# Kernel tuning notes

Hardware: AMD Instinct MI355X
Metric: run time of the kernel (lower is better)

Reference implementation:

```python
import jax, jax.numpy as jnp
import numpy as np

D_MODEL = 2048
D_INNER = 2048
D_XB = 512
N_HEADS = 32
HEADDIM = 64   # P
DSTATE = 64    # N
N_KV = D_XB // DSTATE          # 8 kv heads
REP = N_HEADS // N_KV
D_FF = 8192
DCONV = 4
EPS = 1e-5
B, L = 1, 2048


def _rmsnorm(x, w, eps=EPS):
    return x * jax.lax.rsqrt(jnp.mean(x * x, axis=-1, keepdims=True) + eps) * w


def _silu(x):
    return x * jax.nn.sigmoid(x)


def _causal_dwconv(x, w, b):
    # x: (B,L,C), depthwise causal conv, kernel DCONV
    xp = jnp.pad(x, ((0, 0), (DCONV - 1, 0), (0, 0)))
    y = b
    for k in range(DCONV):  # small fixed kernel loop
        y = y + xp[:, k:k + x.shape[1], :] * w[:, k]
    return y


def setup_inputs() -> dict:
    key = jax.random.key(0)
    ks = jax.random.split(key, 10)
    s = 0.02
    d_proj = 2 * D_INNER + 2 * D_XB + N_HEADS  # z, x, B, C, dt
    conv_ch = 2 * D_XB + D_INNER               # conv over concat(x, B, C)
    return {
        "hidden_states": jax.random.normal(ks[0], (B, L, D_MODEL), jnp.float32),
        "in_proj_w": jax.random.normal(ks[1], (d_proj, D_MODEL), jnp.float32) * s,
        "conv_w": jax.random.normal(ks[2], (conv_ch, DCONV), jnp.float32) * s,
        "conv_b": jnp.zeros((conv_ch,), jnp.float32),
        "dt_bias": jax.random.normal(ks[3], (N_HEADS,), jnp.float32) * s,
        "A_log": jnp.log(jnp.arange(1, N_HEADS + 1, dtype=jnp.float32)),
        "D": jnp.ones((N_HEADS,), jnp.float32),
        "ssm_norm_w": jnp.ones((D_INNER,), jnp.float32),
        "out_proj_w": jax.random.normal(ks[4], (D_MODEL, D_INNER), jnp.float32) * s,
        "input_ln_w": jnp.ones((D_MODEL,), jnp.float32),
        "post_ln_w": jnp.ones((D_MODEL,), jnp.float32),
        "gate_w": jax.random.normal(ks[5], (D_FF, D_MODEL), jnp.float32) * s,
        "up_w": jax.random.normal(ks[6], (D_FF, D_MODEL), jnp.float32) * s,
        "down_w": jax.random.normal(ks[7], (D_MODEL, D_FF), jnp.float32) * s,
    }


def _mamba2(hs, in_proj_w, conv_w, conv_b, dt_bias, A_log, D, ssm_norm_w, out_proj_w):
    b, l, _ = hs.shape
    zxbcdt = hs @ in_proj_w.T
    z, x, Bm, Cm, dt = jnp.split(
        zxbcdt, [D_INNER, D_INNER + D_XB, D_INNER + 2 * D_XB, 2 * D_INNER + 2 * D_XB], axis=-1)
    # causal depthwise conv + silu over concat(x, B, C)
    xBC = _silu(_causal_dwconv(jnp.concatenate([x, Bm, Cm], axis=-1), conv_w, conv_b))
    x, Bm, Cm = jnp.split(xBC, [D_XB, 2 * D_XB], axis=-1)
    # heads (GQA: repeat x and B from N_KV to N_HEADS)
    x = jnp.repeat(x.reshape(b, l, N_KV, HEADDIM), REP, axis=2)      # (b,l,H,P)
    Bm = jnp.repeat(Bm.reshape(b, l, N_KV, DSTATE), REP, axis=2)     # (b,l,H,N)
    Cm = Cm.reshape(b, l, N_HEADS, DSTATE)                            # (b,l,H,N)
    dt = jax.nn.softplus(dt + dt_bias)                                # (b,l,H)
    dA = jnp.exp(dt * (-jnp.exp(A_log)))                              # (b,l,H)
    # selective scan over time
    xs = (jnp.moveaxis(dA, 1, 0), jnp.moveaxis(dt, 1, 0),
          jnp.moveaxis(x, 1, 0), jnp.moveaxis(Bm, 1, 0), jnp.moveaxis(Cm, 1, 0))
    h0 = jnp.zeros((b, N_HEADS, HEADDIM, DSTATE), hs.dtype)

    def step(h, t):
        dA_t, dt_t, x_t, B_t, C_t = t
        h = h * dA_t[:, :, None, None] + jnp.einsum('bh,bhp,bhn->bhpn', dt_t, x_t, B_t)
        y = jnp.einsum('bhpn,bhn->bhp', h, C_t)
        return h, y

    _, ys = jax.lax.scan(step, h0, xs)            # (l,b,H,P)
    y = jnp.moveaxis(ys, 0, 1) + D[None, None, :, None] * x
    y = y.reshape(b, l, D_INNER)
    y = _rmsnorm(y * _silu(z), ssm_norm_w)        # gated RMSNorm
    return y @ out_proj_w.T


def reference(hidden_states, in_proj_w, conv_w, conv_b, dt_bias, A_log, D,
              ssm_norm_w, out_proj_w, input_ln_w, post_ln_w, gate_w, up_w, down_w):
    residual = hidden_states
    h = _rmsnorm(hidden_states, input_ln_w)
    h = residual + _mamba2(h, in_proj_w, conv_w, conv_b, dt_bias, A_log, D,
                           ssm_norm_w, out_proj_w)
    residual = h
    h = _rmsnorm(h, post_ln_w)
    h = (_silu(h @ gate_w.T) * (h @ up_w.T)) @ down_w.T
    return residual + h
```

## Files before the change

kernel.cpp:

```cpp
#include <hip/hip_runtime.h>

typedef unsigned short u16;
typedef unsigned int u32;
typedef float f32x4 __attribute__((ext_vector_type(4)));
typedef __bf16 bf16x8 __attribute__((ext_vector_type(8)));
typedef unsigned short u16x8 __attribute__((ext_vector_type(8)));

#define L_SEQ 2048
#define DMODEL 2048
#define DINNER 2048
#define DXB 512
#define NHEADS 32
#define DPROJ 5152
#define CONVCH 3072
#define DFF 8192
#define NCHUNK 32
#define CHUNK 64

__device__ __forceinline__ float bf2f(u16 u) {
  union { unsigned int i; float f; } v; v.i = ((unsigned int)u) << 16; return v.f;
}
__device__ __forceinline__ u16 f2bf(float f) {
  union { float f; unsigned int i; } v; v.f = f;
  unsigned int u = v.i;
  u += 0x7FFFu + ((u >> 16) & 1u);
  return (u16)(u >> 16);
}
__device__ __forceinline__ float siluf(float x) { return x / (1.f + __expf(-x)); }

#define GL16(gsrc, ldst) \
  __builtin_amdgcn_global_load_lds((const __attribute__((address_space(1))) u32*)(gsrc), \
                                   (__attribute__((address_space(3))) u32*)(ldst), 16, 0, 0)

__global__ __launch_bounds__(256) void cvt_k(
    const float* __restrict__ s, u16* __restrict__ d, int n8)
{
  const int i = blockIdx.x * 256 + threadIdx.x;
  if (i >= n8) return;
  f32x4 a = *(const f32x4*)(s + (size_t)i * 8);
  f32x4 b = *(const f32x4*)(s + (size_t)i * 8 + 4);
  u16x8 o;
#pragma unroll
  for (int j = 0; j < 4; ++j) { o[j] = f2bf(a[j]); o[j + 4] = f2bf(b[j]); }
  *(u16x8*)(d + (size_t)i * 8) = o;
}

template<int EPI, int SPLIT>
__global__ __launch_bounds__(256, 4) void gemm_gl(
    const u16* __restrict__ A, const u16* __restrict__ W,
    void* Cptr, const u16* gateB, int N, int K)
{
  __shared__ u16 Al[128 * 64];
  __shared__ u16 Bl[128 * 64];
  const int tid = threadIdx.x;
  const int w = tid >> 6, ln = tid & 63;
  const int m0 = blockIdx.y << 7, n0 = blockIdx.x << 7;
  const int steps = (K >> 6) / SPLIT;
  const int kt0 = blockIdx.z * steps;

  const int lrow = ln >> 3;
  const int lcol = (ln & 7) << 3;

  f32x4 acc[4][4];
#pragma unroll
  for (int i = 0; i < 4; ++i)
#pragma unroll
    for (int j = 0; j < 4; ++j) acc[i][j] = f32x4{0.f, 0.f, 0.f, 0.f};

  const int wr = w >> 1, wc = w & 1;
  const int lr = ln & 15;
  const int lk = (ln >> 4) << 3;

  for (int kt = kt0; kt < kt0 + steps; ++kt) {
    const int kc = (kt << 6) + lcol;
#pragma unroll
    for (int i = 0; i < 4; ++i) {
      const int r = w * 32 + i * 8;
      GL16(A + (size_t)(m0 + r + lrow) * K + kc, &Al[r * 64]);
      int rw = n0 + r + lrow; rw = rw < N ? rw : N - 1;
      GL16(W + (size_t)rw * K + kc, &Bl[r * 64]);
    }
    __syncthreads();
    bf16x8 af[4], bfr[4];
#pragma unroll
    for (int kk = 0; kk < 2; ++kk) {
#pragma unroll
      for (int m = 0; m < 4; ++m)
        af[m] = *(const bf16x8*)&Al[(wr * 64 + m * 16 + lr) * 64 + kk * 32 + lk];
#pragma unroll
      for (int n = 0; n < 4; ++n)
        bfr[n] = *(const bf16x8*)&Bl[(wc * 64 + n * 16 + lr) * 64 + kk * 32 + lk];
#pragma unroll
      for (int m = 0; m < 4; ++m)
#pragma unroll
        for (int n = 0; n < 4; ++n)
          acc[m][n] = __builtin_amdgcn_mfma_f32_16x16x32_bf16(af[m], bfr[n], acc[m][n], 0, 0, 0);
    }
    __syncthreads();
  }

  const int colb = n0 + (wc << 6) + lr;
  const int rowb = m0 + (wr << 6) + ((ln >> 4) << 2);
#pragma unroll
  for (int m = 0; m < 4; ++m) {
#pragma unroll
    for (int n = 0; n < 4; ++n) {
      const int col = colb + (n << 4);
      if (col < N) {
#pragma unroll
        for (int j = 0; j < 4; ++j) {
          const size_t idx = (size_t)(rowb + (m << 4) + j) * N + col;
          if (EPI == 0) {
            ((u16*)Cptr)[idx] = f2bf(acc[m][n][j]);
          } else if (EPI == 2) {
            float* P = (float*)Cptr + (size_t)blockIdx.z * ((size_t)L_SEQ * N);
            P[idx] = acc[m][n][j];
          } else {
            const float g = bf2f(gateB[idx]);
            ((u16*)Cptr)[idx] = f2bf(siluf(g) * acc[m][n][j]);
          }
        }
      }
    }
  }
}

__global__ __launch_bounds__(256) void rmsnorm_k(
    const float* __restrict__ in, const float* __restrict__ w, u16* __restrict__ out)
{
  const int row = blockIdx.x, tid = threadIdx.x;
  const float* r = in + (size_t)row * DMODEL + tid * 8;
  f32x4 v0 = *(const f32x4*)r;
  f32x4 v1 = *(const f32x4*)(r + 4);
  float ss = v0[0]*v0[0] + v0[1]*v0[1] + v0[2]*v0[2] + v0[3]*v0[3]
           + v1[0]*v1[0] + v1[1]*v1[1] + v1[2]*v1[2] + v1[3]*v1[3];
#pragma unroll
  for (int off = 1; off < 64; off <<= 1) ss += __shfl_xor(ss, off);
  __shared__ float part[4];
  if ((tid & 63) == 0) part[tid >> 6] = ss;
  __syncthreads();
  const float tot = part[0] + part[1] + part[2] + part[3];
  const float scale = rsqrtf(tot * (1.f / DMODEL) + 1e-5f);
  f32x4 w0 = *(const f32x4*)(w + tid * 8);
  f32x4 w1 = *(const f32x4*)(w + tid * 8 + 4);
  u16x8 o;
#pragma unroll
  for (int j = 0; j < 4; ++j) {
    o[j]     = f2bf(v0[j] * scale * w0[j]);
    o[j + 4] = f2bf(v1[j] * scale * w1[j]);
  }
  *(u16x8*)(out + (size_t)row * DMODEL + tid * 8) = o;
}

__global__ __launch_bounds__(256) void red4_rms_k(
    const float* __restrict__ P, const float* __restrict__ resid,
    float* __restrict__ hres, const float* __restrict__ w, u16* __restrict__ h2)
{
  const int row = blockIdx.x, tid = threadIdx.x;
  const size_t base = (size_t)row * DMODEL + tid * 8;
  const size_t stride = (size_t)L_SEQ * DMODEL;
  f32x4 v0 = *(const f32x4*)(resid + base);
  f32x4 v1 = *(const f32x4*)(resid + base + 4);
#pragma unroll
  for (int p = 0; p < 4; ++p) {
    v0 += *(const f32x4*)(P + p * stride + base);
    v1 += *(const f32x4*)(P + p * stride + base + 4);
  }
  *(f32x4*)(hres + base) = v0;
  *(f32x4*)(hres + base + 4) = v1;
  float ss = v0[0]*v0[0] + v0[1]*v0[1] + v0[2]*v0[2] + v0[3]*v0[3]
           + v1[0]*v1[0] + v1[1]*v1[1] + v1[2]*v1[2] + v1[3]*v1[3];
#pragma unroll
  for (int off = 1; off < 64; off <<= 1) ss += __shfl_xor(ss, off);
  __shared__ float part[4];
  if ((tid & 63) == 0) part[tid >> 6] = ss;
  __syncthreads();
  const float tot = part[0] + part[1] + part[2] + part[3];
  const float scale = rsqrtf(tot * (1.f / DMODEL) + 1e-5f);
  f32x4 w0 = *(const f32x4*)(w + tid * 8);
  f32x4 w1 = *(const f32x4*)(w + tid * 8 + 4);
  u16x8 o;
#pragma unroll
  for (int j = 0; j < 4; ++j) {
    o[j]     = f2bf(v0[j] * scale * w0[j]);
    o[j + 4] = f2bf(v1[j] * scale * w1[j]);
  }
  *(u16x8*)(h2 + base) = o;
}

__global__ __launch_bounds__(256) void red4_add_k(
    const float* __restrict__ P, const float* __restrict__ resid, float* __restrict__ out)
{
  const size_t base = ((size_t)blockIdx.x * 256 + threadIdx.x) * 8;
  const size_t stride = (size_t)L_SEQ * DMODEL;
  f32x4 v0 = *(const f32x4*)(resid + base);
  f32x4 v1 = *(const f32x4*)(resid + base + 4);
#pragma unroll
  for (int p = 0; p < 4; ++p) {
    v0 += *(const f32x4*)(P + p * stride + base);
    v1 += *(const f32x4*)(P + p * stride + base + 4);
  }
  *(f32x4*)(out + base) = v0;
  *(f32x4*)(out + base + 4) = v1;
}

__global__ __launch_bounds__(256) void gated_rms_k(
    const float* __restrict__ y, const u16* __restrict__ zx,
    const float* __restrict__ w, u16* __restrict__ out)
{
  const int row = blockIdx.x, tid = threadIdx.x;
  const float* yr = y + (size_t)row * DINNER + tid * 8;
  f32x4 y0 = *(const f32x4*)yr;
  f32x4 y1 = *(const f32x4*)(yr + 4);
  u16x8 zv = *(const u16x8*)(zx + (size_t)row * DPROJ + tid * 8);
  float val[8];
#pragma unroll
  for (int j = 0; j < 4; ++j) {
    val[j]     = y0[j] * siluf(bf2f(zv[j]));
    val[j + 4] = y1[j] * siluf(bf2f(zv[j + 4]));
  }
  float ss = 0.f;
#pragma unroll
  for (int j = 0; j < 8; ++j) ss += val[j] * val[j];
#pragma unroll
  for (int off = 1; off < 64; off <<= 1) ss += __shfl_xor(ss, off);
  __shared__ float part[4];
  if ((tid & 63) == 0) part[tid >> 6] = ss;
  __syncthreads();
  const float tot = part[0] + part[1] + part[2] + part[3];
  const float scale = rsqrtf(tot * (1.f / DINNER) + 1e-5f);
  u16x8 o;
#pragma unroll
  for (int j = 0; j < 8; ++j) o[j] = f2bf(val[j] * scale * w[tid * 8 + j]);
  *(u16x8*)(out + (size_t)row * DINNER + tid * 8) = o;
}

__global__ __launch_bounds__(256) void conv_k(
    const u16* __restrict__ zx, const float* __restrict__ w,
    const float* __restrict__ b, u16* __restrict__ xbc)
{
  const int flat = blockIdx.x * 256 + threadIdx.x;
  const int t = flat / 384;
  const int c8 = (flat % 384) * 8;
  float acc[8];
  f32x4 b0 = *(const f32x4*)(b + c8);
  f32x4 b1 = *(const f32x4*)(b + c8 + 4);
#pragma unroll
  for (int j = 0; j < 4; ++j) { acc[j] = b0[j]; acc[j + 4] = b1[j]; }
  f32x4 wr[8];
#pragma unroll
  for (int j = 0; j < 8; ++j) wr[j] = *(const f32x4*)(w + (size_t)(c8 + j) * 4);
#pragma unroll
  for (int k = 0; k < 4; ++k) {
    const int tt = t - 3 + k;
    if (tt >= 0) {
      u16x8 xv = *(const u16x8*)(zx + (size_t)tt * DPROJ + DINNER + c8);
#pragma unroll
      for (int j = 0; j < 8; ++j) acc[j] += bf2f(xv[j]) * wr[j][k];
    }
  }
  u16x8 o;
#pragma unroll
  for (int j = 0; j < 8; ++j) o[j] = f2bf(siluf(acc[j]));
  *(u16x8*)(xbc + (size_t)t * CONVCH + c8) = o;
}

__global__ __launch_bounds__(256) void dt_k(
    const u16* __restrict__ zx, const float* __restrict__ dt_bias,
    const float* __restrict__ A_log, float* __restrict__ dtv, float* __restrict__ dAv)
{
  const int flat = blockIdx.x * 256 + threadIdx.x;
  const int t = flat >> 5, h = flat & 31;
  const float x = bf2f(zx[(size_t)t * DPROJ + (DPROJ - NHEADS) + h]) + dt_bias[h];
  const float sp = (x > 20.f) ? x : log1pf(expf(x));
  const float a = expf(A_log[h]);
  dtv[flat] = sp;
  dAv[flat] = expf(-a * sp);
}

__device__ __forceinline__ void stage16(float* dst, const u16* src) {
  u16x8 a = *(const u16x8*)src;
  u16x8 b = *(const u16x8*)(src + 8);
#pragma unroll
  for (int j = 0; j < 8; ++j) { dst[j] = bf2f(a[j]); dst[8 + j] = bf2f(b[j]); }
}

__global__ __launch_bounds__(256) void scan_a(
    const u16* __restrict__ xbc, const float* __restrict__ dtv,
    const float* __restrict__ dAv, const float* __restrict__ Dvec,
    float* __restrict__ y, float* __restrict__ S,
    float* __restrict__ gam, float* __restrict__ cum)
{
  __shared__ float xs[64][64], Bs[64][64], Cs[64][64];
  __shared__ float dts[64], dAs[64];
  const int c = blockIdx.x, h = blockIdx.y, kv = h >> 2;
  const int tid = threadIdx.x;
  const int t0 = c * CHUNK;
  {
    const int r = tid >> 2, cq = (tid & 3) * 16;
    const u16* base = xbc + (size_t)(t0 + r) * CONVCH;
    stage16(&xs[r][cq], base + kv * 64 + cq);
    stage16(&Bs[r][cq], base + DXB + kv * 64 + cq);
    stage16(&Cs[r][cq], base + 2 * DXB + h * 64 + cq);
    if (tid < 64) {
      dts[tid] = dtv[(size_t)(t0 + tid) * NHEADS + h];
      dAs[tid] = dAv[(size_t)(t0 + tid) * NHEADS + h];
    }
  }
  __syncthreads();
  const int p = tid >> 2, q = tid & 3;
  float hreg[16];
#pragma unroll
  for (int i = 0; i < 16; ++i) hreg[i] = 0.f;
  float cumv = 1.f;
  const float Dh = Dvec[h];
  for (int t = 0; t < CHUNK; ++t) {
    const float dtt = dts[t], dat = dAs[t];
    const float xv = xs[t][p];
    const float u = dtt * xv;
    float a0 = 0.f, a1 = 0.f, a2 = 0.f, a3 = 0.f;
#pragma unroll
    for (int i4 = 0; i4 < 4; ++i4) {
      f32x4 b4 = *(const f32x4*)&Bs[t][q * 16 + i4 * 4];
      f32x4 c4 = *(const f32x4*)&Cs[t][q * 16 + i4 * 4];
#pragma unroll
      for (int j = 0; j < 4; ++j) {
        const int i = i4 * 4 + j;
        hreg[i] = hreg[i] * dat + u * b4[j];
        if (i4 == 0) a0 += hreg[i] * c4[j];
        else if (i4 == 1) a1 += hreg[i] * c4[j];
        else if (i4 == 2) a2 += hreg[i] * c4[j];
        else a3 += hreg[i] * c4[j];
      }
    }
    float accv = (a0 + a1) + (a2 + a3);
    accv += __shfl_xor(accv, 1);
    accv += __shfl_xor(accv, 2);
    cumv *= dat;
    if (q == 0) y[(size_t)(t0 + t) * DINNER + h * 64 + p] = accv + Dh * xv;
    if (tid == 0) cum[(size_t)(t0 + t) * NHEADS + h] = cumv;
  }
  float* Sp = S + ((size_t)(c * NHEADS + h) << 12) + tid * 16;
#pragma unroll
  for (int i4 = 0; i4 < 4; ++i4)
    *(f32x4*)(Sp + i4 * 4) = f32x4{hreg[i4*4], hreg[i4*4+1], hreg[i4*4+2], hreg[i4*4+3]};
  if (tid == 0) gam[c * NHEADS + h] = cumv;
}

__global__ __launch_bounds__(256) void scan_b(
    const float* __restrict__ S, const float* __restrict__ gam, float* __restrict__ H)
{
  const int h = blockIdx.x, tid = threadIdx.x;
  float hr[16];
#pragma unroll
  for (int i = 0; i < 16; ++i) hr[i] = 0.f;
  for (int c = 0; c < NCHUNK; ++c) {
    const size_t base = ((size_t)(c * NHEADS + h) << 12) + tid * 16;
#pragma unroll
    for (int i4 = 0; i4 < 4; ++i4)
      *(f32x4*)(H + base + i4 * 4) = f32x4{hr[i4*4], hr[i4*4+1], hr[i4*4+2], hr[i4*4+3]};
    const float g = gam[c * NHEADS + h];
#pragma unroll
    for (int i4 = 0; i4 < 4; ++i4) {
      f32x4 s = *(const f32x4*)(S + base + i4 * 4);
#pragma unroll
      for (int j = 0; j < 4; ++j) hr[i4 * 4 + j] = g * hr[i4 * 4 + j] + s[j];
    }
  }
}

__global__ __launch_bounds__(256) void scan_c(
    const u16* __restrict__ xbc, const float* __restrict__ cum,
    const float* __restrict__ H, float* __restrict__ y)
{
  __shared__ float Cs[64][64];
  __shared__ float cums[64];
  const int c = blockIdx.x, h = blockIdx.y, tid = threadIdx.x;
  const int t0 = c * CHUNK;
  {
    const int r = tid >> 2, cq = (tid & 3) * 16;
    stage16(&Cs[r][cq], xbc + (size_t)(t0 + r) * CONVCH + 2 * DXB + h * 64 + cq);
    if (tid < 64) cums[tid] = cum[(size_t)(t0 + tid) * NHEADS + h];
  }
  const int p = tid >> 2, q = tid & 3;
  float hr[16];
  const size_t base = ((size_t)(c * NHEADS + h) << 12) + tid * 16;
#pragma unroll
  for (int i4 = 0; i4 < 4; ++i4) {
    f32x4 v = *(const f32x4*)(H + base + i4 * 4);
#pragma unroll
    for (int j = 0; j < 4; ++j) hr[i4 * 4 + j] = v[j];
  }
  __syncthreads();
  for (int t = 0; t < CHUNK; ++t) {
    float accv = 0.f;
#pragma unroll
    for (int i4 = 0; i4 < 4; ++i4) {
      f32x4 c4 = *(const f32x4*)&Cs[t][q * 16 + i4 * 4];
#pragma unroll
      for (int j = 0; j < 4; ++j) accv += hr[i4 * 4 + j] * c4[j];
    }
    accv += __shfl_xor(accv, 1);
    accv += __shfl_xor(accv, 2);
    if (q == 0) {
      const size_t idx = (size_t)(t0 + t) * DINNER + h * 64 + p;
      y[idx] += cums[t] * accv;
    }
  }
}

extern "C" void kernel_launch(void* const* d_in, const int* in_sizes, int n_in,
                              void* d_out, int out_size, void* d_ws, size_t ws_size,
                              hipStream_t stream) {
  const float* hs         = (const float*)d_in[0];
  const float* in_proj_w  = (const float*)d_in[1];
  const float* conv_w     = (const float*)d_in[2];
  const float* conv_b     = (const float*)d_in[3];
  const float* dt_bias    = (const float*)d_in[4];
  const float* A_log      = (const float*)d_in[5];
  const float* Dv         = (const float*)d_in[6];
  const float* ssm_w      = (const float*)d_in[7];
  const float* out_proj_w = (const float*)d_in[8];
  const float* in_ln_w    = (const float*)d_in[9];
  const float* post_ln_w  = (const float*)d_in[10];
  const float* gate_w     = (const float*)d_in[11];
  const float* up_w       = (const float*)d_in[12];
  const float* down_w     = (const float*)d_in[13];
  float* out = (float*)d_out;

  char* ws = (char*)d_ws;
  size_t off = 0;
  auto alloc = [&](size_t bytes) -> void* {
    void* p = ws + off;
    off = (off + bytes + 255) & ~(size_t)255;
    return p;
  };
  u16* wip = (u16*)alloc((size_t)DPROJ  * DMODEL * 2);
  u16* wop = (u16*)alloc((size_t)DMODEL * DINNER * 2);
  u16* wg  = (u16*)alloc((size_t)DFF    * DMODEL * 2);
  u16* wu  = (u16*)alloc((size_t)DFF    * DMODEL * 2);
  u16* wd  = (u16*)alloc((size_t)DMODEL * DFF    * 2);
  u16*   zx  = (u16*)  alloc((size_t)L_SEQ * DPROJ * 2);
  u16*   xbc = (u16*)  alloc((size_t)L_SEQ * CONVCH * 2);
  float* Sv  = (float*)alloc((size_t)NCHUNK * NHEADS * 4096 * 4);
  float* Hv  = (float*)alloc((size_t)NCHUNK * NHEADS * 4096 * 4);
  float* pK  = (float*)zx;
  float* dtv = (float*)alloc((size_t)L_SEQ * NHEADS * 4);
  float* dAv = (float*)alloc((size_t)L_SEQ * NHEADS * 4);
  float* cum = (float*)alloc((size_t)L_SEQ * NHEADS * 4);
  float* gam = (float*)alloc((size_t)NCHUNK * NHEADS * 4);
  float* yv  = (float*)alloc((size_t)L_SEQ * DINNER * 4);
  float* hres= (float*)alloc((size_t)L_SEQ * DMODEL * 4);
  u16*  gateb= (u16*)  alloc((size_t)L_SEQ * DFF * 2);
  u16*  hslot= (u16*)  alloc((size_t)L_SEQ * DMODEL * 2);
  (void)ws_size; (void)in_sizes; (void)n_in; (void)out_size;

  cvt_k<<<(DPROJ * DMODEL / 8 + 255) / 256, 256, 0, stream>>>(in_proj_w, wip, DPROJ * DMODEL / 8);
  cvt_k<<<DMODEL * DINNER / 8 / 256, 256, 0, stream>>>(out_proj_w, wop, DMODEL * DINNER / 8);
  cvt_k<<<DFF * DMODEL / 8 / 256, 256, 0, stream>>>(gate_w, wg, DFF * DMODEL / 8);
  cvt_k<<<DFF * DMODEL / 8 / 256, 256, 0, stream>>>(up_w, wu, DFF * DMODEL / 8);
  cvt_k<<<DMODEL * DFF / 8 / 256, 256, 0, stream>>>(down_w, wd, DMODEL * DFF / 8);

  rmsnorm_k<<<L_SEQ, 256, 0, stream>>>(hs, in_ln_w, hslot);
  gemm_gl<0, 1><<<dim3(41, 16, 1), 256, 0, stream>>>(hslot, wip, zx, nullptr, DPROJ, DMODEL);
  conv_k<<<(L_SEQ * (CONVCH / 8)) / 256, 256, 0, stream>>>(zx, conv_w, conv_b, xbc);
  dt_k<<<(L_SEQ * NHEADS) / 256, 256, 0, stream>>>(zx, dt_bias, A_log, dtv, dAv);
  scan_a<<<dim3(NCHUNK, NHEADS), 256, 0, stream>>>(xbc, dtv, dAv, Dv, yv, Sv, gam, cum);
  scan_b<<<NHEADS, 256, 0, stream>>>(Sv, gam, Hv);
  scan_c<<<dim3(NCHUNK, NHEADS), 256, 0, stream>>>(xbc, cum, Hv, yv);
  gated_rms_k<<<L_SEQ, 256, 0, stream>>>(yv, zx, ssm_w, hslot);
  gemm_gl<2, 4><<<dim3(16, 16, 4), 256, 0, stream>>>(hslot, wop, pK, nullptr, DMODEL, DINNER);
  red4_rms_k<<<L_SEQ, 256, 0, stream>>>(pK, hs, hres, post_ln_w, hslot);
  gemm_gl<0, 1><<<dim3(64, 16, 1), 256, 0, stream>>>(hslot, wg, gateb, nullptr, DFF, DMODEL);
  gemm_gl<3, 1><<<dim3(64, 16, 1), 256, 0, stream>>>(hslot, wu, gateb, gateb, DFF, DMODEL);
  gemm_gl<2, 4><<<dim3(16, 16, 4), 256, 0, stream>>>(gateb, wd, pK, nullptr, DMODEL, DFF);
  red4_add_k<<<(L_SEQ * DMODEL / 8) / 256, 256, 0, stream>>>(pK, hres, out);
}
```

Before: 604.5 us.

## Replace GEMM with 256x256 double-buffered 8-wave pipelined kernel

Replaces the 128x128 single-buffered GEMM with a 256x256-tile, 512-thread kernel. It double-buffers LDS with global_load_lds, swizzles LDS columns to avoid bank conflicts, interleaves quarter-tile MFMA bursts with the next stage's loads using explicit waitcnt, barriers and setprio, and remaps workgroups across XCDs. The in_proj weight is zero-padded to a multiple of 256 rows so the loader needs no clamping. The aim is to hide global-load latency and raise MFMA utilisation in the GEMMs that dominate runtime. The cost is a large LDS footprint, lower occupancy, and fewer workgroups for the smaller GEMMs, which risks under-filling the GPU.

```diff
diff --git a/kernel.cpp b/kernel.cpp
--- a/kernel.cpp
+++ b/kernel.cpp
@@ -12,6 +12,7 @@
 #define DXB 512
 #define NHEADS 32
 #define DPROJ 5152
+#define DPROJ_PAD 5376
 #define CONVCH 3072
 #define DFF 8192
 #define NCHUNK 32
@@ -31,6 +32,11 @@
 #define GL16(gsrc, ldst) \
   __builtin_amdgcn_global_load_lds((const __attribute__((address_space(1))) u32*)(gsrc), \
                                    (__attribute__((address_space(3))) u32*)(ldst), 16, 0, 0)
+#define SBAR() __builtin_amdgcn_s_barrier()
+#define SCHED0() __builtin_amdgcn_sched_barrier(0)
+#define WAIT_LGKM0() do { asm volatile("s_waitcnt lgkmcnt(0)" ::: "memory"); SCHED0(); } while (0)
+#define WAIT_VM4() asm volatile("s_waitcnt vmcnt(4)" ::: "memory")
+#define WAIT_VM0() asm volatile("s_waitcnt vmcnt(0)" ::: "memory")
 
 __global__ __launch_bounds__(256) void cvt_k(
     const float* __restrict__ s, u16* __restrict__ d, int n8)
@@ -45,79 +51,185 @@
   *(u16x8*)(d + (size_t)i * 8) = o;
 }
 
+__global__ __launch_bounds__(256) void cvt_pad_k(
+    const float* __restrict__ s, u16* __restrict__ d)
+{
+  const int i = blockIdx.x * 256 + threadIdx.x;
+  const int row = (i * 8) >> 11;
+  u16x8 o;
+  if (row < DPROJ) {
+    f32x4 a = *(const f32x4*)(s + (size_t)i * 8);
+    f32x4 b = *(const f32x4*)(s + (size_t)i * 8 + 4);
+#pragma unroll
+    for (int j = 0; j < 4; ++j) { o[j] = f2bf(a[j]); o[j + 4] = f2bf(b[j]); }
+  } else {
+#pragma unroll
+    for (int j = 0; j < 8; ++j) o[j] = 0;
+  }
+  *(u16x8*)(d + (size_t)i * 8) = o;
+}
+
+template<int MH, int NH>
+__device__ __forceinline__ void mfma16(f32x4 (&acc)[8][4], const bf16x8 (&af)[4][2],
+                                       const bf16x8 (&bf)[2][2]) {
+#pragma unroll
+  for (int m = 0; m < 4; ++m)
+#pragma unroll
+    for (int n = 0; n < 2; ++n)
+#pragma unroll
+      for (int s = 0; s < 2; ++s)
+        acc[MH * 4 + m][NH * 2 + n] = __builtin_amdgcn_mfma_f32_16x16x32_bf16(
+            af[m][s], bf[n][s], acc[MH * 4 + m][NH * 2 + n], 0, 0, 0);
+}
+
 template<int EPI, int SPLIT>
-__global__ __launch_bounds__(256, 4) void gemm_gl(
+__global__ __launch_bounds__(512, 2) void gemm8(
     const u16* __restrict__ A, const u16* __restrict__ W,
-    void* Cptr, const u16* gateB, int N, int K)
-{
-  __shared__ u16 Al[128 * 64];
-  __shared__ u16 Bl[128 * 64];
+    void* __restrict__ Cptr, const u16* __restrict__ gateB,
+    const int N, const int K, const int gx)
+{
+  __shared__ u16 sm[65536];
   const int tid = threadIdx.x;
-  const int w = tid >> 6, ln = tid & 63;
-  const int m0 = blockIdx.y << 7, n0 = blockIdx.x << 7;
-  const int steps = (K >> 6) / SPLIT;
-  const int kt0 = blockIdx.z * steps;
-
-  const int lrow = ln >> 3;
-  const int lcol = (ln & 7) << 3;
-
-  f32x4 acc[4][4];
-#pragma unroll
-  for (int i = 0; i < 4; ++i)
+  const int wid = tid >> 6, ln = tid & 63;
+  const int wm = wid >> 2, wn = wid & 3;
+
+  const int nwg = gridDim.x;
+  int wg = (int)blockIdx.x;
+  wg = (wg & 7) * (nwg >> 3) + (wg >> 3);
+  const int tilesPerZ = gx * 8;
+  const int bz = wg / tilesPerZ;
+  const int rem = wg - bz * tilesPerZ;
+  const int by = rem / gx;
+  const int bx = rem - by * gx;
+  const int m0 = by << 8, n0 = bx << 8;
+  const int NT = (K >> 6) / SPLIT;
+  const int ktB = bz * NT;
+
+  f32x4 acc[8][4];
+#pragma unroll
+  for (int i = 0; i < 8; ++i)
 #pragma unroll
     for (int j = 0; j < 4; ++j) acc[i][j] = f32x4{0.f, 0.f, 0.f, 0.f};
 
-  const int wr = w >> 1, wc = w & 1;
-  const int lr = ln & 15;
-  const int lk = (ln >> 4) << 3;
-
-  for (int kt = kt0; kt < kt0 + steps; ++kt) {
-    const int kc = (kt << 6) + lcol;
-#pragma unroll
-    for (int i = 0; i < 4; ++i) {
-      const int r = w * 32 + i * 8;
-      GL16(A + (size_t)(m0 + r + lrow) * K + kc, &Al[r * 64]);
-      int rw = n0 + r + lrow; rw = rw < N ? rw : N - 1;
-      GL16(W + (size_t)rw * K + kc, &Bl[r * 64]);
-    }
-    __syncthreads();
-    bf16x8 af[4], bfr[4];
-#pragma unroll
-    for (int kk = 0; kk < 2; ++kk) {
-#pragma unroll
-      for (int m = 0; m < 4; ++m)
-        af[m] = *(const bf16x8*)&Al[(wr * 64 + m * 16 + lr) * 64 + kk * 32 + lk];
-#pragma unroll
-      for (int n = 0; n < 4; ++n)
-        bfr[n] = *(const bf16x8*)&Bl[(wc * 64 + n * 16 + lr) * 64 + kk * 32 + lk];
-#pragma unroll
-      for (int m = 0; m < 4; ++m)
-#pragma unroll
-        for (int n = 0; n < 4; ++n)
-          acc[m][n] = __builtin_amdgcn_mfma_f32_16x16x32_bf16(af[m], bfr[n], acc[m][n], 0, 0, 0);
-    }
-    __syncthreads();
-  }
-
-  const int colb = n0 + (wc << 6) + lr;
-  const int rowb = m0 + (wr << 6) + ((ln >> 4) << 2);
-#pragma unroll
-  for (int m = 0; m < 4; ++m) {
+  const int l8r = ln >> 3;
+  const int schunk = (ln & 7) ^ l8r;
+  const int lr16 = ln & 15;
+  const int q4 = ln >> 4;
+  const int swz = ln & 7;
+  const int c0 = ((q4 ^ swz) << 3);
+
+  auto stageA = [&](int buf, int kt, int h) {
+#pragma unroll
+    for (int g = 0; g < 2; ++g) {
+      const int rr = (wid << 3) + l8r;
+      const size_t grow = (size_t)(m0 + (g << 7) + (h << 6) + rr);
+      const u16* src = A + grow * K + (size_t)((ktB + kt) << 6) + (schunk << 3);
+      u16* dst = &sm[(buf << 15) + (((h << 7) + (g << 6) + (wid << 3)) << 6)];
+      GL16(src, dst);
+    }
+  };
+  auto stageB = [&](int buf, int kt, int h) {
+#pragma unroll
+    for (int g = 0; g < 2; ++g) {
+      const int v = (g << 6) + (wid << 3) + l8r;
+      const int grow = n0 + ((v >> 5) << 6) + (h << 5) + (v & 31);
+      const u16* src = W + (size_t)grow * K + (size_t)((ktB + kt) << 6) + (schunk << 3);
+      u16* dst = &sm[(buf << 15) + 16384 + (((h << 7) + (g << 6) + (wid << 3)) << 6)];
+      GL16(src, dst);
+    }
+  };
+
+  bf16x8 af[4][2], bf[2][2];
+  auto loadA = [&](int buf, int mh) {
+#pragma unroll
+    for (int m = 0; m < 4; ++m) {
+      const int lrA = (mh << 7) + (wm << 6) + (m << 4) + lr16;
+      const u16* p = &sm[(buf << 15) + (lrA << 6)];
+      af[m][0] = *(const bf16x8*)(p + c0);
+      af[m][1] = *(const bf16x8*)(p + (c0 ^ 32));
+    }
+  };
+  auto loadB = [&](int buf, int nh) {
+#pragma unroll
+    for (int n = 0; n < 2; ++n) {
+      const int lrB = (nh << 7) + (wn << 5) + (n << 4) + lr16;
+      const u16* p = &sm[(buf << 15) + 16384 + (lrB << 6)];
+      bf[n][0] = *(const bf16x8*)(p + c0);
+      bf[n][1] = *(const bf16x8*)(p + (c0 ^ 32));
+    }
+  };
+
+  stageA(0, 0, 0); stageA(0, 0, 1); stageB(0, 0, 0); stageB(0, 0, 1);
+  stageA(1, 1, 0); stageB(1, 1, 1);
+  WAIT_VM4();
+  SBAR();
+
+  for (int kt = 0; kt < NT; kt += 2) {
+    const bool s2 = (kt + 2) < NT, s3 = (kt + 3) < NT;
+    loadA(0, 0); loadB(0, 0);
+    stageA(1, kt + 1, 1);
+    SBAR(); WAIT_LGKM0();
+    __builtin_amdgcn_s_setprio(1); mfma16<0, 0>(acc, af, bf); __builtin_amdgcn_s_setprio(0);
+    SCHED0(); SBAR();
+    loadB(0, 1);
+    stageB(1, kt + 1, 0);
+    SBAR(); WAIT_LGKM0();
+    __builtin_amdgcn_s_setprio(1); mfma16<0, 1>(acc, af, bf); __builtin_amdgcn_s_setprio(0);
+    SCHED0(); SBAR();
+    loadA(0, 1);
+    if (s2) stageA(0, kt + 2, 0);
+    SBAR(); WAIT_LGKM0();
+    __builtin_amdgcn_s_setprio(1); mfma16<1, 1>(acc, af, bf); __builtin_amdgcn_s_setprio(0);
+    SCHED0(); SBAR();
+    loadB(0, 0);
+    if (s2) stageB(0, kt + 2, 1);
+    SBAR(); WAIT_LGKM0();
+    __builtin_amdgcn_s_setprio(1); mfma16<1, 0>(acc, af, bf); __builtin_amdgcn_s_setprio(0);
+    SCHED0();
+    if (s2) { WAIT_VM4(); } else { WAIT_VM0(); }
+    SBAR();
+    loadA(1, 0); loadB(1, 0);
+    if (s2) stageA(0, kt + 2, 1);
+    SBAR(); WAIT_LGKM0();
+    __builtin_amdgcn_s_setprio(1); mfma16<0, 0>(acc, af, bf); __builtin_amdgcn_s_setprio(0);
+    SCHED0(); SBAR();
+    loadB(1, 1);
+    if (s2) stageB(0, kt + 2, 0);
+    SBAR(); WAIT_LGKM0();
+    __builtin_amdgcn_s_setprio(1); mfma16<0, 1>(acc, af, bf); __builtin_amdgcn_s_setprio(0);
+    SCHED0(); SBAR();
+    loadA(1, 1);
+    if (s3) stageA(1, kt + 3, 0);
+    SBAR(); WAIT_LGKM0();
+    __builtin_amdgcn_s_setprio(1); mfma16<1, 1>(acc, af, bf); __builtin_amdgcn_s_setprio(0);
+    SCHED0(); SBAR();
+    loadB(1, 0);
+    if (s3) stageB(1, kt + 3, 1);
+    SBAR(); WAIT_LGKM0();
+    __builtin_amdgcn_s_setprio(1); mfma16<1, 0>(acc, af, bf); __builtin_amdgcn_s_setprio(0);
+    SCHED0();
+    if (s2) { if (s3) { WAIT_VM4(); } else { WAIT_VM0(); } }
+    SBAR();
+  }
+
+  const int crow0 = m0 + (wm << 7) + (q4 << 2);
+  const int ccol0 = n0 + (wn << 6) + lr16;
+#pragma unroll
+  for (int M = 0; M < 8; ++M) {
 #pragma unroll
     for (int n = 0; n < 4; ++n) {
-      const int col = colb + (n << 4);
+      const int col = ccol0 + (n << 4);
       if (col < N) {
 #pragma unroll
         for (int j = 0; j < 4; ++j) {
-          const size_t idx = (size_t)(rowb + (m << 4) + j) * N + col;
+          const size_t idx = (size_t)(crow0 + (M << 4) + j) * N + col;
           if (EPI == 0) {
-            ((u16*)Cptr)[idx] = f2bf(acc[m][n][j]);
+            ((u16*)Cptr)[idx] = f2bf(acc[M][n][j]);
           } else if (EPI == 2) {
-            float* P = (float*)Cptr + (size_t)blockIdx.z * ((size_t)L_SEQ * N);
-            P[idx] = acc[m][n][j];
+            float* P = (float*)Cptr + (size_t)bz * ((size_t)L_SEQ * N);
+            P[idx] = acc[M][n][j];
           } else {
-            const float g = bf2f(gateB[idx]);
-            ((u16*)Cptr)[idx] = f2bf(siluf(g) * acc[m][n][j]);
+            ((u16*)Cptr)[idx] = f2bf(siluf(bf2f(gateB[idx])) * acc[M][n][j]);
           }
         }
       }
@@ -435,7 +547,7 @@
     off = (off + bytes + 255) & ~(size_t)255;
     return p;
   };
-  u16* wip = (u16*)alloc((size_t)DPROJ  * DMODEL * 2);
+  u16* wip = (u16*)alloc((size_t)DPROJ_PAD * DMODEL * 2);
   u16* wop = (u16*)alloc((size_t)DMODEL * DINNER * 2);
   u16* wg  = (u16*)alloc((size_t)DFF    * DMODEL * 2);
   u16* wu  = (u16*)alloc((size_t)DFF    * DMODEL * 2);
@@ -455,24 +567,24 @@
   u16*  hslot= (u16*)  alloc((size_t)L_SEQ * DMODEL * 2);
   (void)ws_size; (void)in_sizes; (void)n_in; (void)out_size;
 
-  cvt_k<<<(DPROJ * DMODEL / 8 + 255) / 256, 256, 0, stream>>>(in_proj_w, wip, DPROJ * DMODEL / 8);
+  cvt_pad_k<<<(DPROJ_PAD * DMODEL / 8) / 256, 256, 0, stream>>>(in_proj_w, wip);
   cvt_k<<<DMODEL * DINNER / 8 / 256, 256, 0, stream>>>(out_proj_w, wop, DMODEL * DINNER / 8);
   cvt_k<<<DFF * DMODEL / 8 / 256, 256, 0, stream>>>(gate_w, wg, DFF * DMODEL / 8);
   cvt_k<<<DFF * DMODEL / 8 / 256, 256, 0, stream>>>(up_w, wu, DFF * DMODEL / 8);
   cvt_k<<<DMODEL * DFF / 8 / 256, 256, 0, stream>>>(down_w, wd, DMODEL * DFF / 8);
 
   rmsnorm_k<<<L_SEQ, 256, 0, stream>>>(hs, in_ln_w, hslot);
-  gemm_gl<0, 1><<<dim3(41, 16, 1), 256, 0, stream>>>(hslot, wip, zx, nullptr, DPROJ, DMODEL);
+  gemm8<0, 1><<<21 * 8, 512, 0, stream>>>(hslot, wip, zx, nullptr, DPROJ, DMODEL, 21);
   conv_k<<<(L_SEQ * (CONVCH / 8)) / 256, 256, 0, stream>>>(zx, conv_w, conv_b, xbc);
   dt_k<<<(L_SEQ * NHEADS) / 256, 256, 0, stream>>>(zx, dt_bias, A_log, dtv, dAv);
   scan_a<<<dim3(NCHUNK, NHEADS), 256, 0, stream>>>(xbc, dtv, dAv, Dv, yv, Sv, gam, cum);
   scan_b<<<NHEADS, 256, 0, stream>>>(Sv, gam, Hv);
   scan_c<<<dim3(NCHUNK, NHEADS), 256, 0, stream>>>(xbc, cum, Hv, yv);
   gated_rms_k<<<L_SEQ, 256, 0, stream>>>(yv, zx, ssm_w, hslot);
-  gemm_gl<2, 4><<<dim3(16, 16, 4), 256, 0, stream>>>(hslot, wop, pK, nullptr, DMODEL, DINNER);
+  gemm8<2, 4><<<8 * 8 * 4, 512, 0, stream>>>(hslot, wop, pK, nullptr, DMODEL, DINNER, 8);
   red4_rms_k<<<L_SEQ, 256, 0, stream>>>(pK, hs, hres, post_ln_w, hslot);
-  gemm_gl<0, 1><<<dim3(64, 16, 1), 256, 0, stream>>>(hslot, wg, gateb, nullptr, DFF, DMODEL);
-  gemm_gl<3, 1><<<dim3(64, 16, 1), 256, 0, stream>>>(hslot, wu, gateb, gateb, DFF, DMODEL);
-  gemm_gl<2, 4><<<dim3(16, 16, 4), 256, 0, stream>>>(gateb, wd, pK, nullptr, DMODEL, DFF);
+  gemm8<0, 1><<<32 * 8, 512, 0, stream>>>(hslot, wg, gateb, nullptr, DFF, DMODEL, 32);
+  gemm8<3, 1><<<32 * 8, 512, 0, stream>>>(hslot, wu, gateb, gateb, DFF, DMODEL, 32);
+  gemm8<2, 4><<<8 * 8 * 4, 512, 0, stream>>>(gateb, wd, pK, nullptr, DMODEL, DFF, 8);
   red4_add_k<<<(L_SEQ * DMODEL / 8) / 256, 256, 0, stream>>>(pK, hres, out);
 }
```

Result: faster. 538.6 us (-10.9%).

## Swizzle GEMM LDS tiles, remap blocks across XCDs, fuse conv/dt, widen scan_b

Applied to the files above, without the earlier changes.

The GEMM kernel now XOR-swizzles the 16-byte column chunks in LDS so that MFMA fragment reads avoid bank conflicts. It also launches a 1D grid that is remapped so consecutive tiles land on the same XCD, aiming for better L2 reuse. The in_proj weight is zero-padded to a multiple of 128 rows, which removes the row clamp in the load path at the cost of a slightly larger conversion. The conv and dt kernels are merged into one launch. scan_b now uses one thread per state element across 512 blocks instead of 32 blocks, giving it much more parallelism.

```diff
diff --git a/kernel.cpp b/kernel.cpp
--- a/kernel.cpp
+++ b/kernel.cpp
@@ -12,6 +12,7 @@
 #define DXB 512
 #define NHEADS 32
 #define DPROJ 5152
+#define DPROJ_PAD 5376
 #define CONVCH 3072
 #define DFF 8192
 #define NCHUNK 32
@@ -45,21 +46,47 @@
   *(u16x8*)(d + (size_t)i * 8) = o;
 }
 
+__global__ __launch_bounds__(256) void cvt_pad_k(
+    const float* __restrict__ s, u16* __restrict__ d)
+{
+  const int i = blockIdx.x * 256 + threadIdx.x;
+  const int row = (i * 8) >> 11;
+  u16x8 o;
+  if (row < DPROJ) {
+    f32x4 a = *(const f32x4*)(s + (size_t)i * 8);
+    f32x4 b = *(const f32x4*)(s + (size_t)i * 8 + 4);
+#pragma unroll
+    for (int j = 0; j < 4; ++j) { o[j] = f2bf(a[j]); o[j + 4] = f2bf(b[j]); }
+  } else {
+#pragma unroll
+    for (int j = 0; j < 8; ++j) o[j] = 0;
+  }
+  *(u16x8*)(d + (size_t)i * 8) = o;
+}
+
 template<int EPI, int SPLIT>
-__global__ __launch_bounds__(256, 4) void gemm_gl(
+__global__ __launch_bounds__(256) void gemm128(
     const u16* __restrict__ A, const u16* __restrict__ W,
-    void* Cptr, const u16* gateB, int N, int K)
+    void* __restrict__ Cptr, const u16* __restrict__ gateB,
+    const int N, const int K, const int gx)
 {
   __shared__ u16 Al[128 * 64];
   __shared__ u16 Bl[128 * 64];
   const int tid = threadIdx.x;
   const int w = tid >> 6, ln = tid & 63;
-  const int m0 = blockIdx.y << 7, n0 = blockIdx.x << 7;
-  const int steps = (K >> 6) / SPLIT;
-  const int kt0 = blockIdx.z * steps;
-
-  const int lrow = ln >> 3;
-  const int lcol = (ln & 7) << 3;
+  const int wr = w >> 1, wc = w & 1;
+
+  const int nwg = gridDim.x;
+  int wg = (int)blockIdx.x;
+  wg = (wg & 7) * (nwg >> 3) + (wg >> 3);
+  const int tilesPerZ = gx << 4;
+  const int bz = wg / tilesPerZ;
+  const int rem = wg - bz * tilesPerZ;
+  const int bx = rem >> 4;
+  const int by = rem & 15;
+  const int m0 = by << 7, n0 = bx << 7;
+  const int NT = (K >> 6) / SPLIT;
+  const int ktB = bz * NT;
 
   f32x4 acc[4][4];
 #pragma unroll
@@ -67,29 +94,35 @@
 #pragma unroll
     for (int j = 0; j < 4; ++j) acc[i][j] = f32x4{0.f, 0.f, 0.f, 0.f};
 
-  const int wr = w >> 1, wc = w & 1;
-  const int lr = ln & 15;
-  const int lk = (ln >> 4) << 3;
-
-  for (int kt = kt0; kt < kt0 + steps; ++kt) {
-    const int kc = (kt << 6) + lcol;
+  const int l8r = ln >> 3;
+  const int schunk = (ln & 7) ^ l8r;
+  const int lr16 = ln & 15;
+  const int q4 = ln >> 4;
+  const int rswz = lr16 & 7;
+
+  for (int kt = ktB; kt < ktB + NT; ++kt) {
+    const size_t kcol = ((size_t)kt << 6) + (schunk << 3);
 #pragma unroll
     for (int i = 0; i < 4; ++i) {
-      const int r = w * 32 + i * 8;
-      GL16(A + (size_t)(m0 + r + lrow) * K + kc, &Al[r * 64]);
-      int rw = n0 + r + lrow; rw = rw < N ? rw : N - 1;
-      GL16(W + (size_t)rw * K + kc, &Bl[r * 64]);
+      const int r = (w << 5) + (i << 3);
+      GL16(A + (size_t)(m0 + r + l8r) * K + kcol, &Al[r << 6]);
+      GL16(W + (size_t)(n0 + r + l8r) * K + kcol, &Bl[r << 6]);
     }
     __syncthreads();
-    bf16x8 af[4], bfr[4];
 #pragma unroll
     for (int kk = 0; kk < 2; ++kk) {
-#pragma unroll
-      for (int m = 0; m < 4; ++m)
-        af[m] = *(const bf16x8*)&Al[(wr * 64 + m * 16 + lr) * 64 + kk * 32 + lk];
-#pragma unroll
-      for (int n = 0; n < 4; ++n)
-        bfr[n] = *(const bf16x8*)&Bl[(wc * 64 + n * 16 + lr) * 64 + kk * 32 + lk];
+      bf16x8 af[4], bfr[4];
+      const int ch = (kk << 2) + q4;
+#pragma unroll
+      for (int m = 0; m < 4; ++m) {
+        const int rA = (wr << 6) + (m << 4) + lr16;
+        af[m] = *(const bf16x8*)&Al[(rA << 6) + ((ch ^ rswz) << 3)];
+      }
+#pragma unroll
+      for (int n = 0; n < 4; ++n) {
+        const int rB = (wc << 6) + (n << 4) + lr16;
+        bfr[n] = *(const bf16x8*)&Bl[(rB << 6) + ((ch ^ rswz) << 3)];
+      }
 #pragma unroll
       for (int m = 0; m < 4; ++m)
 #pragma unroll
@@ -99,8 +132,8 @@
     __syncthreads();
   }
 
-  const int colb = n0 + (wc << 6) + lr;
-  const int rowb = m0 + (wr << 6) + ((ln >> 4) << 2);
+  const int colb = n0 + (wc << 6) + lr16;
+  const int rowb = m0 + (wr << 6) + (q4 << 2);
 #pragma unroll
   for (int m = 0; m < 4; ++m) {
 #pragma unroll
@@ -113,11 +146,10 @@
           if (EPI == 0) {
             ((u16*)Cptr)[idx] = f2bf(acc[m][n][j]);
           } else if (EPI == 2) {
-            float* P = (float*)Cptr + (size_t)blockIdx.z * ((size_t)L_SEQ * N);
+            float* P = (float*)Cptr + (size_t)bz * ((size_t)L_SEQ * N);
             P[idx] = acc[m][n][j];
           } else {
-            const float g = bf2f(gateB[idx]);
-            ((u16*)Cptr)[idx] = f2bf(siluf(g) * acc[m][n][j]);
+            ((u16*)Cptr)[idx] = f2bf(siluf(bf2f(gateB[idx])) * acc[m][n][j]);
           }
         }
       }
@@ -235,47 +267,46 @@
   *(u16x8*)(out + (size_t)row * DINNER + tid * 8) = o;
 }
 
-__global__ __launch_bounds__(256) void conv_k(
+__global__ __launch_bounds__(256) void convdt_k(
     const u16* __restrict__ zx, const float* __restrict__ w,
-    const float* __restrict__ b, u16* __restrict__ xbc)
-{
-  const int flat = blockIdx.x * 256 + threadIdx.x;
-  const int t = flat / 384;
-  const int c8 = (flat % 384) * 8;
-  float acc[8];
-  f32x4 b0 = *(const f32x4*)(b + c8);
-  f32x4 b1 = *(const f32x4*)(b + c8 + 4);
-#pragma unroll
-  for (int j = 0; j < 4; ++j) { acc[j] = b0[j]; acc[j + 4] = b1[j]; }
-  f32x4 wr[8];
-#pragma unroll
-  for (int j = 0; j < 8; ++j) wr[j] = *(const f32x4*)(w + (size_t)(c8 + j) * 4);
-#pragma unroll
-  for (int k = 0; k < 4; ++k) {
-    const int tt = t - 3 + k;
-    if (tt >= 0) {
-      u16x8 xv = *(const u16x8*)(zx + (size_t)tt * DPROJ + DINNER + c8);
-#pragma unroll
-      for (int j = 0; j < 8; ++j) acc[j] += bf2f(xv[j]) * wr[j][k];
-    }
-  }
-  u16x8 o;
-#pragma unroll
-  for (int j = 0; j < 8; ++j) o[j] = f2bf(siluf(acc[j]));
-  *(u16x8*)(xbc + (size_t)t * CONVCH + c8) = o;
-}
-
-__global__ __launch_bounds__(256) void dt_k(
-    const u16* __restrict__ zx, const float* __restrict__ dt_bias,
-    const float* __restrict__ A_log, float* __restrict__ dtv, float* __restrict__ dAv)
-{
-  const int flat = blockIdx.x * 256 + threadIdx.x;
-  const int t = flat >> 5, h = flat & 31;
-  const float x = bf2f(zx[(size_t)t * DPROJ + (DPROJ - NHEADS) + h]) + dt_bias[h];
-  const float sp = (x > 20.f) ? x : log1pf(expf(x));
-  const float a = expf(A_log[h]);
-  dtv[flat] = sp;
-  dAv[flat] = expf(-a * sp);
+    const float* __restrict__ b, u16* __restrict__ xbc,
+    const float* __restrict__ dt_bias, const float* __restrict__ A_log,
+    float* __restrict__ dtv, float* __restrict__ dAv)
+{
+  if (blockIdx.x < 3072) {
+    const int flat = blockIdx.x * 256 + threadIdx.x;
+    const int t = flat / 384;
+    const int c8 = (flat % 384) * 8;
+    float acc[8];
+    f32x4 b0 = *(const f32x4*)(b + c8);
+    f32x4 b1 = *(const f32x4*)(b + c8 + 4);
+#pragma unroll
+    for (int j = 0; j < 4; ++j) { acc[j] = b0[j]; acc[j + 4] = b1[j]; }
+    f32x4 wr[8];
+#pragma unroll
+    for (int j = 0; j < 8; ++j) wr[j] = *(const f32x4*)(w + (size_t)(c8 + j) * 4);
+#pragma unroll
+    for (int k = 0; k < 4; ++k) {
+      const int tt = t - 3 + k;
+      if (tt >= 0) {
+        u16x8 xv = *(const u16x8*)(zx + (size_t)tt * DPROJ + DINNER + c8);
+#pragma unroll
+        for (int j = 0; j < 8; ++j) acc[j] += bf2f(xv[j]) * wr[j][k];
+      }
+    }
+    u16x8 o;
+#pragma unroll
+    for (int j = 0; j < 8; ++j) o[j] = f2bf(siluf(acc[j]));
+    *(u16x8*)(xbc + (size_t)t * CONVCH + c8) = o;
+  } else {
+    const int flat = (blockIdx.x - 3072) * 256 + threadIdx.x;
+    const int t = flat >> 5, h = flat & 31;
+    const float x = bf2f(zx[(size_t)t * DPROJ + (DPROJ - NHEADS) + h]) + dt_bias[h];
+    const float sp = (x > 20.f) ? x : log1pf(expf(x));
+    const float a = expf(A_log[h]);
+    dtv[flat] = sp;
+    dAv[flat] = expf(-a * sp);
+  }
 }
 
 __device__ __forceinline__ void stage16(float* dst, const u16* src) {
@@ -350,22 +381,14 @@
 __global__ __launch_bounds__(256) void scan_b(
     const float* __restrict__ S, const float* __restrict__ gam, float* __restrict__ H)
 {
-  const int h = blockIdx.x, tid = threadIdx.x;
-  float hr[16];
-#pragma unroll
-  for (int i = 0; i < 16; ++i) hr[i] = 0.f;
+  const int g = blockIdx.x * 256 + threadIdx.x;
+  const int h = g >> 12;
+  const int e = g & 4095;
+  float hr = 0.f;
   for (int c = 0; c < NCHUNK; ++c) {
-    const size_t base = ((size_t)(c * NHEADS + h) << 12) + tid * 16;
-#pragma unroll
-    for (int i4 = 0; i4 < 4; ++i4)
-      *(f32x4*)(H + base + i4 * 4) = f32x4{hr[i4*4], hr[i4*4+1], hr[i4*4+2], hr[i4*4+3]};
-    const float g = gam[c * NHEADS + h];
-#pragma unroll
-    for (int i4 = 0; i4 < 4; ++i4) {
-      f32x4 s = *(const f32x4*)(S + base + i4 * 4);
-#pragma unroll
-      for (int j = 0; j < 4; ++j) hr[i4 * 4 + j] = g * hr[i4 * 4 + j] + s[j];
-    }
+    const size_t base = (((size_t)(c * NHEADS + h)) << 12) + e;
+    H[base] = hr;
+    hr = gam[c * NHEADS + h] * hr + S[base];
   }
 }
 
@@ -435,7 +458,7 @@
     off = (off + bytes + 255) & ~(size_t)255;
     return p;
   };
-  u16* wip = (u16*)alloc((size_t)DPROJ  * DMODEL * 2);
+  u16* wip = (u16*)alloc((size_t)DPROJ_PAD * DMODEL * 2);
   u16* wop = (u16*)alloc((size_t)DMODEL * DINNER * 2);
   u16* wg  = (u16*)alloc((size_t)DFF    * DMODEL * 2);
   u16* wu  = (u16*)alloc((size_t)DFF    * DMODEL * 2);
@@ -455,24 +478,23 @@
   u16*  hslot= (u16*)  alloc((size_t)L_SEQ * DMODEL * 2);
   (void)ws_size; (void)in_sizes; (void)n_in; (void)out_size;
 
-  cvt_k<<<(DPROJ * DMODEL / 8 + 255) / 256, 256, 0, stream>>>(in_proj_w, wip, DPROJ * DMODEL / 8);
+  cvt_pad_k<<<(DPROJ_PAD * DMODEL / 8) / 256, 256, 0, stream>>>(in_proj_w, wip);
   cvt_k<<<DMODEL * DINNER / 8 / 256, 256, 0, stream>>>(out_proj_w, wop, DMODEL * DINNER / 8);
   cvt_k<<<DFF * DMODEL / 8 / 256, 256, 0, stream>>>(gate_w, wg, DFF * DMODEL / 8);
   cvt_k<<<DFF * DMODEL / 8 / 256, 256, 0, stream>>>(up_w, wu, DFF * DMODEL / 8);
   cvt_k<<<DMODEL * DFF / 8 / 256, 256, 0, stream>>>(down_w, wd, DMODEL * DFF / 8);
 
   rmsnorm_k<<<L_SEQ, 256, 0, stream>>>(hs, in_ln_w, hslot);
-  gemm_gl<0, 1><<<dim3(41, 16, 1), 256, 0, stream>>>(hslot, wip, zx, nullptr, DPROJ, DMODEL);
-  conv_k<<<(L_SEQ * (CONVCH / 8)) / 256, 256, 0, stream>>>(zx, conv_w, conv_b, xbc);
-  dt_k<<<(L_SEQ * NHEADS) / 256, 256, 0, stream>>>(zx, dt_bias, A_log, dtv, dAv);
+  gemm128<0, 1><<<41 * 16, 256, 0, stream>>>(hslot, wip, zx, nullptr, DPROJ, DMODEL, 41);
+  convdt_k<<<3072 + 256, 256, 0, stream>>>(zx, conv_w, conv_b, xbc, dt_bias, A_log, dtv, dAv);
   scan_a<<<dim3(NCHUNK, NHEADS), 256, 0, stream>>>(xbc, dtv, dAv, Dv, yv, Sv, gam, cum);
-  scan_b<<<NHEADS, 256, 0, stream>>>(Sv, gam, Hv);
+  scan_b<<<512, 256, 0, stream>>>(Sv, gam, Hv);
   scan_c<<<dim3(NCHUNK, NHEADS), 256, 0, stream>>>(xbc, cum, Hv, yv);
   gated_rms_k<<<L_SEQ, 256, 0, stream>>>(yv, zx, ssm_w, hslot);
-  gemm_gl<2, 4><<<dim3(16, 16, 4), 256, 0, stream>>>(hslot, wop, pK, nullptr, DMODEL, DINNER);
+  gemm128<2, 4><<<16 * 16 * 4, 256, 0, stream>>>(hslot, wop, pK, nullptr, DMODEL, DINNER, 16);
   red4_rms_k<<<L_SEQ, 256, 0, stream>>>(pK, hs, hres, post_ln_w, hslot);
-  gemm_gl<0, 1><<<dim3(64, 16, 1), 256, 0, stream>>>(hslot, wg, gateb, nullptr, DFF, DMODEL);
-  gemm_gl<3, 1><<<dim3(64, 16, 1), 256, 0, stream>>>(hslot, wu, gateb, gateb, DFF, DMODEL);
-  gemm_gl<2, 4><<<dim3(16, 16, 4), 256, 0, stream>>>(gateb, wd, pK, nullptr, DMODEL, DFF);
+  gemm128<0, 1><<<64 * 16, 256, 0, stream>>>(hslot, wg, gateb, nullptr, DFF, DMODEL, 64);
+  gemm128<3, 1><<<64 * 16, 256, 0, stream>>>(hslot, wu, gateb, gateb, DFF, DMODEL, 64);
+  gemm128<2, 4><<<16 * 16 * 4, 256, 0, stream>>>(gateb, wd, pK, nullptr, DMODEL, DFF, 16);
   red4_add_k<<<(L_SEQ * DMODEL / 8) / 256, 256, 0, stream>>>(pK, hres, out);
 }
```

New measurement: 658.8 us. 9.0% more time.
